# Kernel optimization log

Hardware: AMD Instinct MI355X
Metric: run time of the kernel (lower is better)

Reference implementation:

```python
import jax, jax.numpy as jnp
import numpy as np

NUM_HEADS = 8      # in_channels // num_head_channels = 512 // 64
NUM_GROUPS = 32    # GroupNorm groups
EPS = 1e-5


def setup_inputs() -> dict:
    key = jax.random.key(0)
    ks = jax.random.split(key, 6)
    C = 512
    x = jax.random.normal(ks[0], (8, C, 32, 32), dtype=jnp.float32)
    gn_w = jax.random.normal(ks[1], (C,), dtype=jnp.float32) * 0.1 + 1.0
    gn_b = jax.random.normal(ks[2], (C,), dtype=jnp.float32) * 0.1
    qkv_w = jax.random.normal(ks[3], (3 * C, C), dtype=jnp.float32) / np.sqrt(C)
    qkv_b = jnp.zeros((3 * C,), dtype=jnp.float32)
    # NOTE: original zero-initializes to_out; we use small random weights so the
    # attention path contributes to the output (math is identical).
    out_w = jax.random.normal(ks[4], (C, C), dtype=jnp.float32) * 0.02
    out_b = jax.random.normal(ks[5], (C,), dtype=jnp.float32) * 0.02
    return {"x": x, "gn_w": gn_w, "gn_b": gn_b, "qkv_w": qkv_w,
            "qkv_b": qkv_b, "out_w": out_w, "out_b": out_b}


def _group_norm(net, gn_w, gn_b):
    b, c, t = net.shape
    g = net.reshape(b, NUM_GROUPS, c // NUM_GROUPS, t)
    mu = jnp.mean(g, axis=(2, 3), keepdims=True)
    var = jnp.var(g, axis=(2, 3), keepdims=True)
    n = ((g - mu) * jax.lax.rsqrt(var + EPS)).reshape(b, c, t)
    return n * gn_w[None, :, None] + gn_b[None, :, None]


def reference(x, gn_w, gn_b, qkv_w, qkv_b, out_w, out_b):
    b, c, h, w = x.shape
    area = h * w
    inp = x.reshape(b, c, area)                      # [b, c, t]
    n = _group_norm(inp, gn_w, gn_b)
    # 1x1 conv1d == channel GEMM
    qkv = jnp.einsum('oc,bct->bot', qkv_w, n) + qkv_b[None, :, None]  # [b, 3c, t]
    hd = c // NUM_HEADS
    # split_qkv_after_heads: view(b*H, 3*hd, area) then split along channel
    qkv = qkv.reshape(b * NUM_HEADS, 3 * hd, area)
    q, k, v = qkv[:, :hd], qkv[:, hd:2 * hd], qkv[:, 2 * hd:]
    scale = 1.0 / np.sqrt(np.sqrt(hd))               # sqrt-sqrt per-tensor scale
    attn = jnp.einsum('bct,bcs->bts', q * scale, k * scale)  # [bH, t, s]
    prob = jax.nn.softmax(attn, axis=-1)
    net = jnp.einsum('bts,bcs->bct', prob, v).reshape(b, c, area)
    out = jnp.einsum('oc,bct->bot', out_w, net) + out_b[None, :, None]
    return (inp + out).reshape(b, c, h, w)
```

## Files before the change

### kernel.cpp

```cpp
#include <hip/hip_runtime.h>
#include <hip/hip_bf16.h>

typedef __bf16 bf16_t;
typedef __bf16 bf16x8 __attribute__((ext_vector_type(8)));
typedef __bf16 bf16x4 __attribute__((ext_vector_type(4)));
typedef short  s16x4  __attribute__((ext_vector_type(4)));
typedef float  f32x4  __attribute__((ext_vector_type(4)));

#define B_DIM 8
#define C_DIM 512
#define T_DIM 1024
#define NH 8
#define HD 64

#define QSCALE 0.180336880111112f

#define GAS __attribute__((address_space(1)))
#define LAS __attribute__((address_space(3)))

__device__ __forceinline__ f32x4 mfma16_bf16(bf16x4 a, bf16x4 b, f32x4 c) {
    return __builtin_amdgcn_mfma_f32_16x16x16bf16_1k(
        __builtin_bit_cast(s16x4, a), __builtin_bit_cast(s16x4, b), c, 0, 0, 0);
}

__device__ __forceinline__ void block_sync_lds() {
    asm volatile("s_waitcnt lgkmcnt(0)" ::: "memory");
    __builtin_amdgcn_s_barrier();
}

__device__ __forceinline__ void stage_sync() {
    asm volatile("s_waitcnt vmcnt(0)" ::: "memory");
    __builtin_amdgcn_s_barrier();
    asm volatile("" ::: "memory");
}

__device__ __forceinline__ void gload_lds16(const bf16_t* g, bf16_t* l) {
    __builtin_amdgcn_global_load_lds((const GAS void*)g, (LAS void*)l, 16, 0, 0);
}

__global__ __launch_bounds__(256) void gn_kernel(const float* __restrict__ x,
                                                 const float* __restrict__ gw,
                                                 const float* __restrict__ gb,
                                                 bf16_t* __restrict__ n_t,
                                                 const float* __restrict__ w1,
                                                 const float* __restrict__ w2,
                                                 bf16_t* __restrict__ o1,
                                                 bf16_t* __restrict__ o2)
{
    __shared__ bf16_t sX[16384];
    __shared__ float sred[8];
    int tid = threadIdx.x;

    if (blockIdx.x >= 256) {
        int tid2 = (blockIdx.x - 256) * 256 + tid;
        for (int p = 0; p < 16; ++p) {
            int q = tid2 + p * 16384;
            const f32x4* src;
            bf16x4* dst;
            int qq;
            if (q < 196608) { src = (const f32x4*)w1; dst = (bf16x4*)o1; qq = q; }
            else            { src = (const f32x4*)w2; dst = (bf16x4*)o2; qq = q - 196608; }
            f32x4 f = src[qq];
            bf16x4 h;
            for (int j = 0; j < 4; ++j) h[j] = (bf16_t)f[j];
            dst[qq] = h;
        }
        return;
    }

    int bb  = blockIdx.x >> 5;
    int g   = blockIdx.x & 31;
    const f32x4* xg4 = reinterpret_cast<const f32x4*>(x + (size_t)(bb * C_DIM + g * 16) * T_DIM);

    float s = 0.f, sq = 0.f;
    for (int i = 0; i < 16; ++i) {
        int v = tid + i * 256;
        f32x4 f = xg4[v];
        bf16x4 h;
        for (int j = 0; j < 4; ++j) {
            s += f[j]; sq += f[j] * f[j];
            h[j] = (bf16_t)f[j];
        }
        *reinterpret_cast<bf16x4*>(sX + v * 4) = h;
    }
    for (int off = 1; off < 64; off <<= 1) {
        s  += __shfl_xor(s, off);
        sq += __shfl_xor(sq, off);
    }
    int wv = tid >> 6;
    if ((tid & 63) == 0) { sred[wv * 2] = s; sred[wv * 2 + 1] = sq; }
    __syncthreads();
    s  = sred[0] + sred[2] + sred[4] + sred[6];
    sq = sred[1] + sred[3] + sred[5] + sred[7];
    float mean = s * (1.f / 16384.f);
    float var  = sq * (1.f / 16384.f) - mean * mean;
    float rs   = rsqrtf(var + 1e-5f);

    int hf = tid & 1;
    float aa[8], bbias[8];
    for (int j = 0; j < 8; ++j) {
        int c = hf * 8 + j;
        float av = gw[g * 16 + c] * rs;
        aa[j] = av;
        bbias[j] = gb[g * 16 + c] - mean * av;
    }
    bf16_t* ob = n_t + (size_t)bb * T_DIM * C_DIM + g * 16 + hf * 8;
    for (int p = 0; p < 8; ++p) {
        int t = (tid >> 1) + p * 128;
        bf16x8 o;
        for (int j = 0; j < 8; ++j) {
            float xv = (float)sX[(hf * 8 + j) * 1024 + t];
            o[j] = (bf16_t)(xv * aa[j] + bbias[j]);
        }
        *reinterpret_cast<bf16x8*>(ob + (size_t)t * C_DIM) = o;
    }
}

__global__ __launch_bounds__(256, 4) void qkv_gemm_kernel(
    const bf16_t* __restrict__ wqb, const float* __restrict__ bq,
    const bf16_t* __restrict__ n_t, bf16_t* __restrict__ qkv)
{
    __shared__ __align__(16) bf16_t smem[16384];
    bf16_t* sA = smem;
    bf16_t* sB = smem + 8192;
    int tid = threadIdx.x;
    int w = tid >> 6, lane = tid & 63, quad = lane >> 4, l15 = lane & 15;
    int bx = blockIdx.x;
    int t0 = blockIdx.y * 128;
    int bb = blockIdx.z;
    int o0 = bx * 128;
    const bf16_t* Ab = wqb + (size_t)o0 * C_DIM;
    const bf16_t* Bb = n_t + ((size_t)bb * T_DIM + t0) * C_DIM;

    f32x4 acc[4][4];
    for (int mt = 0; mt < 4; ++mt)
        for (int nt = 0; nt < 4; ++nt)
            acc[mt][nt] = f32x4{0.f, 0.f, 0.f, 0.f};
    int mw0 = (w >> 1) * 64;
    int nw0 = (w & 1) * 64;

    int srow = (lane >> 3);
    int scol = ((lane & 7) ^ srow) * 8;

    for (int k0 = 0; k0 < C_DIM; k0 += 64) {
        for (int i = 0; i < 4; ++i) {
            int row = i * 32 + w * 8 + srow;
            gload_lds16(Ab + (size_t)row * C_DIM + k0 + scol, sA + i * 2048 + w * 512);
        }
        for (int i = 0; i < 4; ++i) {
            int row = i * 32 + w * 8 + srow;
            gload_lds16(Bb + (size_t)row * C_DIM + k0 + scol, sB + i * 2048 + w * 512);
        }
        stage_sync();
        for (int kk = 0; kk < 2; ++kk) {
            bf16x8 af[4], bfr[4];
            for (int mt = 0; mt < 4; ++mt) {
                int row = mw0 + mt * 16 + l15;
                int cs = kk * 4 + quad;
                af[mt] = *reinterpret_cast<const bf16x8*>(sA + row * 64 + ((cs ^ (row & 7)) << 3));
            }
            for (int nt = 0; nt < 4; ++nt) {
                int row = nw0 + nt * 16 + l15;
                int cs = kk * 4 + quad;
                bfr[nt] = *reinterpret_cast<const bf16x8*>(sB + row * 64 + ((cs ^ (row & 7)) << 3));
            }
            for (int mt = 0; mt < 4; ++mt)
                for (int nt = 0; nt < 4; ++nt)
                    acc[mt][nt] = __builtin_amdgcn_mfma_f32_16x16x32_bf16(af[mt], bfr[nt], acc[mt][nt], 0, 0, 0);
        }
        __builtin_amdgcn_s_barrier();
    }

    bf16_t* es = smem;
    for (int half = 0; half < 2; ++half) {
        int chunk = bx * 2 + half;
        int h = chunk / 3, type = chunk % 3;
        size_t base = ((size_t)(bb * NH + h) * 3 + type) * (64 * 1024);
        bool mine = (mw0 >> 6) == half;

        if (type < 2) {
            float scl = (type == 0) ? QSCALE : 1.0f;
            if (mine)
                for (int mt = 0; mt < 4; ++mt)
                    for (int nt = 0; nt < 4; ++nt)
                        for (int r = 0; r < 4; ++r) {
                            int mw = mt * 16 + quad * 4 + r;
                            int tl = nw0 + nt * 16 + l15;
                            float v = (acc[mt][nt][r] + bq[o0 + half * 64 + mw]) * scl;
                            es[tl * 72 + mw] = (bf16_t)v;
                        }
            __syncthreads();
            for (int i = 0; i < 4; ++i) {
                int v = tid + i * 256;
                int tl = v >> 3, c8 = v & 7;
                bf16x8 d = *reinterpret_cast<const bf16x8*>(es + tl * 72 + c8 * 8);
                *reinterpret_cast<bf16x8*>(qkv + base + (size_t)(t0 + tl) * 64 + c8 * 8) = d;
            }
            __syncthreads();
        } else {
            if (mine)
                for (int mt = 0; mt < 4; ++mt)
                    for (int nt = 0; nt < 4; ++nt)
                        for (int r = 0; r < 4; ++r) {
                            int mw = mt * 16 + quad * 4 + r;
                            int tl = nw0 + nt * 16 + l15;
                            float v = acc[mt][nt][r] + bq[o0 + half * 64 + mw];
                            es[mw * 136 + tl] = (bf16_t)v;
                        }
            __syncthreads();
            for (int i = 0; i < 4; ++i) {
                int v = tid + i * 256;
                int cc = v >> 4, t8 = (v & 15) * 8;
                bf16x8 d = *reinterpret_cast<const bf16x8*>(es + cc * 136 + t8);
                *reinterpret_cast<bf16x8*>(qkv + base + (size_t)cc * 1024 + t0 + t8) = d;
            }
            __syncthreads();
        }
    }
}

__global__ __launch_bounds__(256, 2) void attn_kernel(const bf16_t* __restrict__ qkv,
                                                      bf16_t* __restrict__ net_t)
{
    __shared__ bf16_t sK[4][64 * 72];
    __shared__ bf16_t sV[4][64 * 72];
    int tid = threadIdx.x;
    int w = tid >> 6, lane = tid & 63, quad = lane >> 4, l15 = lane & 15;
    int bh = blockIdx.x;
    int qt = blockIdx.y;
    size_t qb = (size_t)bh * 3 * 65536;
    const bf16_t* Qg = qkv + qb + (size_t)qt * 8192;
    const bf16_t* Kg = qkv + qb + 65536;
    const bf16_t* Vg = qkv + qb + 2 * 65536;

    bf16x8 qf[2][2];
    for (int tt = 0; tt < 2; ++tt)
        for (int kk = 0; kk < 2; ++kk)
            qf[tt][kk] = *reinterpret_cast<const bf16x8*>(
                Qg + (size_t)(tt * 64 + w * 16 + l15) * 64 + kk * 32 + quad * 8);

    int vrow = tid >> 3;
    int vcol = (tid & 7) * 8;

    bf16x8 kA[2], vA[2], kB[2], vB[2];

    auto load_tiles = [&](bf16x8* kr, bf16x8* vr, int s0) {
        for (int i = 0; i < 2; ++i) {
            int r = vrow + i * 32;
            kr[i] = *reinterpret_cast<const bf16x8*>(Kg + (size_t)(s0 + r) * 64 + vcol);
            vr[i] = *reinterpret_cast<const bf16x8*>(Vg + (size_t)r * 1024 + s0 + vcol);
        }
    };
    auto write_tiles = [&](bf16_t* sKb, bf16_t* sVb, const bf16x8* kr, const bf16x8* vr) {
        for (int i = 0; i < 2; ++i) {
            int r = vrow + i * 32;
            *reinterpret_cast<bf16x8*>(sKb + r * 72 + vcol) = kr[i];
            *reinterpret_cast<bf16x8*>(sVb + r * 72 + vcol) = vr[i];
        }
    };

    f32x4 O0[4], O1[4];
    for (int i = 0; i < 4; ++i) {
        O0[i] = f32x4{0.f, 0.f, 0.f, 0.f};
        O1[i] = f32x4{0.f, 0.f, 0.f, 0.f};
    }
    f32x4 L0 = f32x4{0.f, 0.f, 0.f, 0.f};
    f32x4 L1 = f32x4{0.f, 0.f, 0.f, 0.f};
    const bf16x4 kONES = bf16x4{(bf16_t)1.f, (bf16_t)1.f, (bf16_t)1.f, (bf16_t)1.f};

    auto compute_tile = [&](const bf16_t* sKb, const bf16_t* sVb) {
        __builtin_amdgcn_s_setprio(1);
        for (int mt = 0; mt < 4; ++mt) {
            const bf16_t* krow = sKb + (mt * 16 + l15) * 72 + quad * 8;
            bf16x8 kf0 = *reinterpret_cast<const bf16x8*>(krow);
            bf16x8 kf1 = *reinterpret_cast<const bf16x8*>(krow + 32);
            f32x4 S0 = f32x4{0.f, 0.f, 0.f, 0.f};
            f32x4 S1 = f32x4{0.f, 0.f, 0.f, 0.f};
            S0 = __builtin_amdgcn_mfma_f32_16x16x32_bf16(kf0, qf[0][0], S0, 0, 0, 0);
            S1 = __builtin_amdgcn_mfma_f32_16x16x32_bf16(kf0, qf[1][0], S1, 0, 0, 0);
            S0 = __builtin_amdgcn_mfma_f32_16x16x32_bf16(kf1, qf[0][1], S0, 0, 0, 0);
            S1 = __builtin_amdgcn_mfma_f32_16x16x32_bf16(kf1, qf[1][1], S1, 0, 0, 0);
            bf16x4 pf0, pf1;
            for (int r = 0; r < 4; ++r) {
                pf0[r] = (bf16_t)__builtin_amdgcn_exp2f(S0[r]);
                pf1[r] = (bf16_t)__builtin_amdgcn_exp2f(S1[r]);
            }
            L0 = mfma16_bf16(kONES, pf0, L0);
            L1 = mfma16_bf16(kONES, pf1, L1);
            for (int ct = 0; ct < 4; ++ct) {
                bf16x4 vf = *reinterpret_cast<const bf16x4*>(sVb + (ct * 16 + l15) * 72 + mt * 16 + quad * 4);
                O0[ct] = mfma16_bf16(vf, pf0, O0[ct]);
                O1[ct] = mfma16_bf16(vf, pf1, O1[ct]);
            }
        }
        __builtin_amdgcn_s_setprio(0);
    };

    load_tiles(kA, vA, 0);
    load_tiles(kB, vB, 64);
    write_tiles(sK[0], sV[0], kA, vA);
    write_tiles(sK[1], sV[1], kB, vB);
    load_tiles(kA, vA, 128);
    load_tiles(kB, vB, 192);
    block_sync_lds();

    for (int ep = 0; ep < 4; ++ep) {
        write_tiles(sK[2], sV[2], kA, vA);
        write_tiles(sK[3], sV[3], kB, vB);
        if (ep < 3) {
            load_tiles(kA, vA, (4 * ep + 4) * 64);
            load_tiles(kB, vB, (4 * ep + 5) * 64);
        }
        compute_tile(sK[0], sV[0]);
        compute_tile(sK[1], sV[1]);
        block_sync_lds();
        if (ep < 3) {
            write_tiles(sK[0], sV[0], kA, vA);
            write_tiles(sK[1], sV[1], kB, vB);
            load_tiles(kA, vA, (4 * ep + 6) * 64);
            load_tiles(kB, vB, (4 * ep + 7) * 64);
        }
        compute_tile(sK[2], sV[2]);
        compute_tile(sK[3], sV[3]);
        if (ep < 3) block_sync_lds();
    }

    float inv0 = 1.f / L0[0];
    float inv1 = 1.f / L1[0];

    int bb = bh >> 3, h = bh & 7;
    int tbase = qt * 128 + w * 16 + l15;
    bf16_t* orow0 = net_t + ((size_t)bb * T_DIM + tbase) * C_DIM + h * 64;
    bf16_t* orow1 = net_t + ((size_t)bb * T_DIM + tbase + 64) * C_DIM + h * 64;
    for (int ct = 0; ct < 4; ++ct) {
        bf16x4 o4, o5;
        for (int r = 0; r < 4; ++r) {
            o4[r] = (bf16_t)(O0[ct][r] * inv0);
            o5[r] = (bf16_t)(O1[ct][r] * inv1);
        }
        *reinterpret_cast<bf16x4*>(orow0 + ct * 16 + quad * 4) = o4;
        *reinterpret_cast<bf16x4*>(orow1 + ct * 16 + quad * 4) = o5;
    }
}

__global__ __launch_bounds__(256) void out_gemm_kernel(
    const bf16_t* __restrict__ wob, const float* __restrict__ bo,
    const bf16_t* __restrict__ net_t, const float* __restrict__ x,
    float* __restrict__ out)
{
    __shared__ __align__(16) bf16_t smem[12288];
    bf16_t* sA = smem;
    bf16_t* sB = smem + 4096;
    int tid = threadIdx.x;
    int w = tid >> 6, lane = tid & 63, quad = lane >> 4, l15 = lane & 15;
    int o0 = blockIdx.x * 64;
    int t0 = blockIdx.y * 128;
    int bb = blockIdx.z;
    const bf16_t* Ab = wob + (size_t)o0 * C_DIM;
    const bf16_t* Bb = net_t + ((size_t)bb * T_DIM + t0) * C_DIM;

    f32x4 acc[2][4];
    for (int mt = 0; mt < 2; ++mt)
        for (int nt = 0; nt < 4; ++nt)
            acc[mt][nt] = f32x4{0.f, 0.f, 0.f, 0.f};
    int mw0 = (w >> 1) * 32;
    int nw0 = (w & 1) * 64;

    int srow = (lane >> 3);
    int scol = ((lane & 7) ^ srow) * 8;

    for (int k0 = 0; k0 < C_DIM; k0 += 64) {
        for (int i = 0; i < 2; ++i) {
            int row = i * 32 + w * 8 + srow;
            gload_lds16(Ab + (size_t)row * C_DIM + k0 + scol, sA + i * 2048 + w * 512);
        }
        for (int i = 0; i < 4; ++i) {
            int row = i * 32 + w * 8 + srow;
            gload_lds16(Bb + (size_t)row * C_DIM + k0 + scol, sB + i * 2048 + w * 512);
        }
        stage_sync();
        for (int kk = 0; kk < 2; ++kk) {
            bf16x8 af[2], bfr[4];
            for (int mt = 0; mt < 2; ++mt) {
                int row = mw0 + mt * 16 + l15;
                int cs = kk * 4 + quad;
                af[mt] = *reinterpret_cast<const bf16x8*>(sA + row * 64 + ((cs ^ (row & 7)) << 3));
            }
            for (int nt = 0; nt < 4; ++nt) {
                int row = nw0 + nt * 16 + l15;
                int cs = kk * 4 + quad;
                bfr[nt] = *reinterpret_cast<const bf16x8*>(sB + row * 64 + ((cs ^ (row & 7)) << 3));
            }
            for (int mt = 0; mt < 2; ++mt)
                for (int nt = 0; nt < 4; ++nt)
                    acc[mt][nt] = __builtin_amdgcn_mfma_f32_16x16x32_bf16(af[mt], bfr[nt], acc[mt][nt], 0, 0, 0);
        }
        __builtin_amdgcn_s_barrier();
    }

    for (int mt = 0; mt < 2; ++mt)
        for (int nt = 0; nt < 4; ++nt)
            for (int r = 0; r < 4; ++r) {
                int o = o0 + mw0 + mt * 16 + quad * 4 + r;
                int t = t0 + nw0 + nt * 16 + l15;
                size_t idx = ((size_t)bb * C_DIM + o) * T_DIM + t;
                out[idx] = acc[mt][nt][r] + bo[o] + x[idx];
            }
}

extern "C" void kernel_launch(void* const* d_in, const int* in_sizes, int n_in,
                              void* d_out, int out_size, void* d_ws, size_t ws_size,
                              hipStream_t stream)
{
    const float* x     = (const float*)d_in[0];
    const float* gn_w  = (const float*)d_in[1];
    const float* gn_b  = (const float*)d_in[2];
    const float* qkv_w = (const float*)d_in[3];
    const float* qkv_b = (const float*)d_in[4];
    const float* out_w = (const float*)d_in[5];
    const float* out_b = (const float*)d_in[6];
    float* out = (float*)d_out;

    char* ws = (char*)d_ws;
    bf16_t* n_t   = (bf16_t*)(ws);
    bf16_t* qkv   = (bf16_t*)(ws + 8388608);
    bf16_t* net_t = (bf16_t*)(ws + 33554432);
    bf16_t* wqb   = (bf16_t*)(ws + 41943040);
    bf16_t* wob   = (bf16_t*)(ws + 41943040 + 1572864);

    gn_kernel<<<dim3(320), 256, 0, stream>>>(x, gn_w, gn_b, n_t, qkv_w, out_w, wqb, wob);
    qkv_gemm_kernel<<<dim3(12, 8, 8), 256, 0, stream>>>(wqb, qkv_b, n_t, qkv);
    attn_kernel<<<dim3(64, 8), 256, 0, stream>>>(qkv, net_t);
    out_gemm_kernel<<<dim3(8, 8, 8), 256, 0, stream>>>(wob, out_b, net_t, x, out);
}
```

Measured before the change: 145.8 us.

## Stage attention K/V tiles via direct global-to-LDS loads with XOR swizzle

The attention kernel stops loading K/V tiles into registers and writing them to padded shared memory. It now issues global_load_lds 16-byte transfers straight into unpadded LDS buffers and uses an XOR swizzle on columns to avoid bank conflicts. The pipeline becomes a double-buffered pair scheme synchronised with vmcnt waits plus barriers. This cuts register pressure and VGPR-to-LDS store instructions, but the wait points change and the swizzled addressing adds some integer ops.

```diff
diff --git a/kernel.cpp b/kernel.cpp
--- a/kernel.cpp
+++ b/kernel.cpp
@@ -21,11 +21,6 @@
 __device__ __forceinline__ f32x4 mfma16_bf16(bf16x4 a, bf16x4 b, f32x4 c) {
     return __builtin_amdgcn_mfma_f32_16x16x16bf16_1k(
         __builtin_bit_cast(s16x4, a), __builtin_bit_cast(s16x4, b), c, 0, 0, 0);
-}
-
-__device__ __forceinline__ void block_sync_lds() {
-    asm volatile("s_waitcnt lgkmcnt(0)" ::: "memory");
-    __builtin_amdgcn_s_barrier();
 }
 
 __device__ __forceinline__ void stage_sync() {
@@ -222,8 +217,8 @@
 __global__ __launch_bounds__(256, 2) void attn_kernel(const bf16_t* __restrict__ qkv,
                                                       bf16_t* __restrict__ net_t)
 {
-    __shared__ bf16_t sK[4][64 * 72];
-    __shared__ bf16_t sV[4][64 * 72];
+    __shared__ __align__(16) bf16_t sK[4][4096];
+    __shared__ __align__(16) bf16_t sV[4][4096];
     int tid = threadIdx.x;
     int w = tid >> 6, lane = tid & 63, quad = lane >> 4, l15 = lane & 15;
     int bh = blockIdx.x;
@@ -239,23 +234,14 @@
             qf[tt][kk] = *reinterpret_cast<const bf16x8*>(
                 Qg + (size_t)(tt * 64 + w * 16 + l15) * 64 + kk * 32 + quad * 8);
 
-    int vrow = tid >> 3;
-    int vcol = (tid & 7) * 8;
-
-    bf16x8 kA[2], vA[2], kB[2], vB[2];
-
-    auto load_tiles = [&](bf16x8* kr, bf16x8* vr, int s0) {
+    int srow = lane >> 3;
+    int scol = ((lane & 7) ^ srow) * 8;
+
+    auto stage_tile = [&](int b, int s0) {
         for (int i = 0; i < 2; ++i) {
-            int r = vrow + i * 32;
-            kr[i] = *reinterpret_cast<const bf16x8*>(Kg + (size_t)(s0 + r) * 64 + vcol);
-            vr[i] = *reinterpret_cast<const bf16x8*>(Vg + (size_t)r * 1024 + s0 + vcol);
-        }
-    };
-    auto write_tiles = [&](bf16_t* sKb, bf16_t* sVb, const bf16x8* kr, const bf16x8* vr) {
-        for (int i = 0; i < 2; ++i) {
-            int r = vrow + i * 32;
-            *reinterpret_cast<bf16x8*>(sKb + r * 72 + vcol) = kr[i];
-            *reinterpret_cast<bf16x8*>(sVb + r * 72 + vcol) = vr[i];
+            int row = i * 32 + w * 8 + srow;
+            gload_lds16(Kg + (size_t)(s0 + row) * 64 + scol, &sK[b][i * 2048 + w * 512]);
+            gload_lds16(Vg + (size_t)row * 1024 + s0 + scol, &sV[b][i * 2048 + w * 512]);
         }
     };
 
@@ -271,9 +257,10 @@
     auto compute_tile = [&](const bf16_t* sKb, const bf16_t* sVb) {
         __builtin_amdgcn_s_setprio(1);
         for (int mt = 0; mt < 4; ++mt) {
-            const bf16_t* krow = sKb + (mt * 16 + l15) * 72 + quad * 8;
-            bf16x8 kf0 = *reinterpret_cast<const bf16x8*>(krow);
-            bf16x8 kf1 = *reinterpret_cast<const bf16x8*>(krow + 32);
+            int kr = mt * 16 + l15;
+            const bf16_t* kbase = sKb + kr * 64;
+            bf16x8 kf0 = *reinterpret_cast<const bf16x8*>(kbase + ((quad ^ (kr & 7)) << 3));
+            bf16x8 kf1 = *reinterpret_cast<const bf16x8*>(kbase + (((quad + 4) ^ (kr & 7)) << 3));
             f32x4 S0 = f32x4{0.f, 0.f, 0.f, 0.f};
             f32x4 S1 = f32x4{0.f, 0.f, 0.f, 0.f};
             S0 = __builtin_amdgcn_mfma_f32_16x16x32_bf16(kf0, qf[0][0], S0, 0, 0, 0);
@@ -287,8 +274,12 @@
             }
             L0 = mfma16_bf16(kONES, pf0, L0);
             L1 = mfma16_bf16(kONES, pf1, L1);
+            int vslot = mt * 2 + (quad >> 1);
+            int vsub  = (quad & 1) * 4;
             for (int ct = 0; ct < 4; ++ct) {
-                bf16x4 vf = *reinterpret_cast<const bf16x4*>(sVb + (ct * 16 + l15) * 72 + mt * 16 + quad * 4);
+                int vr = ct * 16 + l15;
+                bf16x4 vf = *reinterpret_cast<const bf16x4*>(
+                    sVb + vr * 64 + ((vslot ^ (vr & 7)) << 3) + vsub);
                 O0[ct] = mfma16_bf16(vf, pf0, O0[ct]);
                 O1[ct] = mfma16_bf16(vf, pf1, O1[ct]);
             }
@@ -296,33 +287,23 @@
         __builtin_amdgcn_s_setprio(0);
     };
 
-    load_tiles(kA, vA, 0);
-    load_tiles(kB, vB, 64);
-    write_tiles(sK[0], sV[0], kA, vA);
-    write_tiles(sK[1], sV[1], kB, vB);
-    load_tiles(kA, vA, 128);
-    load_tiles(kB, vB, 192);
-    block_sync_lds();
-
-    for (int ep = 0; ep < 4; ++ep) {
-        write_tiles(sK[2], sV[2], kA, vA);
-        write_tiles(sK[3], sV[3], kB, vB);
-        if (ep < 3) {
-            load_tiles(kA, vA, (4 * ep + 4) * 64);
-            load_tiles(kB, vB, (4 * ep + 5) * 64);
-        }
-        compute_tile(sK[0], sV[0]);
-        compute_tile(sK[1], sV[1]);
-        block_sync_lds();
-        if (ep < 3) {
-            write_tiles(sK[0], sV[0], kA, vA);
-            write_tiles(sK[1], sV[1], kB, vB);
-            load_tiles(kA, vA, (4 * ep + 6) * 64);
-            load_tiles(kB, vB, (4 * ep + 7) * 64);
-        }
-        compute_tile(sK[2], sV[2]);
-        compute_tile(sK[3], sV[3]);
-        if (ep < 3) block_sync_lds();
+    stage_tile(0, 0);
+    stage_tile(1, 64);
+    stage_sync();
+    stage_tile(2, 128);
+    stage_tile(3, 192);
+
+    for (int st2 = 0; st2 < 8; ++st2) {
+        int p = (st2 & 1) * 2;
+        compute_tile(sK[p],     sV[p]);
+        compute_tile(sK[p + 1], sV[p + 1]);
+        if (st2 < 7) {
+            stage_sync();
+            if (st2 < 6) {
+                stage_tile(p,     (2 * st2 + 4) * 64);
+                stage_tile(p + 1, (2 * st2 + 5) * 64);
+            }
+        }
     }
 
     float inv0 = 1.f / L0[0];
```

New measurement: 148.4 us. No clear change (+1.8%).
